# Kernel tuning notes

Hardware: AMD Instinct MI355X
Metric: run time of the kernel (lower is better)

Reference implementation:

```python
import jax, jax.numpy as jnp
import numpy as np
import math

N = 50000
E = 800000
D_IN, D_HID, D_OUT = 128, 64, 64
NUM_LAYERS = 8
ALPHA, THETA = 0.1, 0.5


def setup_inputs() -> dict:
    key = jax.random.key(0)
    ks = jax.random.split(key, 8)
    x = jax.random.normal(ks[0], (N, D_IN), dtype=jnp.float32)
    edge_index = jax.random.randint(ks[1], (2, E), 0, N, dtype=jnp.int64)
    s = 1.0 / np.sqrt(D_HID)
    W0 = jax.random.normal(ks[2], (D_IN, D_HID), dtype=jnp.float32) / np.sqrt(D_IN)
    b0 = jnp.zeros((D_HID,), dtype=jnp.float32)
    Ws = jax.random.normal(ks[3], (NUM_LAYERS, D_HID, D_HID), dtype=jnp.float32) * s
    W_out = jax.random.normal(ks[4], (D_HID, D_OUT), dtype=jnp.float32) * s
    b_out = jnp.zeros((D_OUT,), dtype=jnp.float32)
    return {"x": x, "edge_index": edge_index, "W0": W0, "b0": b0,
            "Ws": Ws, "W_out": W_out, "b_out": b_out}


def reference(x, edge_index, W0, b0, Ws, W_out, b_out):
    n = x.shape[0]
    # GCN normalization with self-loops (PyG gcn_norm, add_self_loops=True)
    loop = jnp.arange(n, dtype=edge_index.dtype)
    src = jnp.concatenate([edge_index[0], loop])
    dst = jnp.concatenate([edge_index[1], loop])
    ones = jnp.ones(src.shape[0], dtype=x.dtype)
    deg = jax.ops.segment_sum(ones, dst, num_segments=n)
    dinv = jnp.where(deg > 0, deg ** -0.5, 0.0)
    norm = (dinv[src] * dinv[dst])[:, None]  # [E+N, 1]

    def propagate(h):
        # out[i] = sum_{(j->i)} norm_ji * h[j]
        return jax.ops.segment_sum(norm * h[src], dst, num_segments=n)

    h = jax.nn.relu(x @ W0 + b0)
    h0 = h
    for layer in range(NUM_LAYERS):
        beta = math.log(THETA / (layer + 1) + 1.0)
        ah = propagate(h)
        xx = (1.0 - ALPHA) * ah + ALPHA * h0          # residual to x_0
        h = (1.0 - beta) * xx + beta * (xx @ Ws[layer])  # identity-mapped linear (shared weights)
        h = jax.nn.relu(h)
    return h @ W_out + b_out
```

## Files before the change

kernel.cpp:

```cpp
#include <hip/hip_runtime.h>
#include <hip/hip_fp16.h>
#include <math.h>

#define NN 50000
#define NE 800000
#define NLAYERS 8
#define NTILE (NN / 16)
#define EPB (NE / 256)
#define NBUCKB ((NN + 255) / 256)
#define BCAP 5120
#define CSRCAP 512

typedef _Float16 f16x8 __attribute__((ext_vector_type(8)));
typedef float f32x4 __attribute__((ext_vector_type(4)));


__global__ __launch_bounds__(256) void k_hist(const int* __restrict__ ei,
                                              int* __restrict__ gh) {
    __shared__ int h[256];
    h[threadIdx.x] = 0;
    __syncthreads();
    int base = blockIdx.x * EPB;
    for (int i = threadIdx.x; i < EPB; i += 256) {
        int d = __builtin_nontemporal_load(ei + NE + base + i);
        atomicAdd(&h[d >> 8], 1);
    }
    __syncthreads();
    gh[blockIdx.x * 256 + threadIdx.x] = h[threadIdx.x];
}

__global__ void k_scanhist(int* __restrict__ gh, int* __restrict__ bbase) {
    __shared__ int tot[256];
    int t = threadIdx.x;
    int run = 0;
    for (int blk = 0; blk < 256; blk++) {
        int v = gh[blk * 256 + t];
        gh[blk * 256 + t] = run;
        run += v;
    }
    tot[t] = run;
    __syncthreads();
    for (int off = 1; off < 256; off <<= 1) {
        int u = (t >= off) ? tot[t - off] : 0;
        __syncthreads();
        tot[t] += u;
        __syncthreads();
    }
    int ebase = tot[t] - run;
    for (int blk = 0; blk < 256; blk++) gh[blk * 256 + t] += ebase;
    bbase[t] = ebase;
    if (t == 255) bbase[256] = NE;
}

__global__ __launch_bounds__(256) void k_part(const int* __restrict__ ei,
                                              const int* __restrict__ gh,
                                              int2* __restrict__ part) {
    __shared__ int lcnt[256];
    int t = threadIdx.x;
    lcnt[t] = gh[blockIdx.x * 256 + t];
    __syncthreads();
    int base = blockIdx.x * EPB;
    for (int i = t; i < EPB; i += 256) {
        int s = __builtin_nontemporal_load(ei + base + i);
        int d = __builtin_nontemporal_load(ei + NE + base + i);
        int pos = atomicAdd(&lcnt[d >> 8], 1);
        int2 e; e.x = s; e.y = d;
        part[pos] = e;
    }
}

__global__ __launch_bounds__(256) void k_bsort(const int2* __restrict__ part,
                                               const int* __restrict__ bbase,
                                               int* __restrict__ csrs,
                                               int* __restrict__ offs,
                                               float* __restrict__ dinv,
                                               float* __restrict__ rdinv) {
    __shared__ int ssrc[BCAP];
    __shared__ unsigned char sdlo[BCAP];
    __shared__ int dcnt[256], dpos[256], scan[256];
    int b = blockIdx.x, t = threadIdx.x;
    int base0 = bbase[b], base1 = bbase[b + 1];
    int n = base1 - base0;
    if (n > BCAP) n = BCAP;
    dcnt[t] = 0;
    __syncthreads();
    for (int i = t; i < n; i += 256) {
        int2 e = part[base0 + i];
        ssrc[i] = e.x;
        int dlo = e.y & 255;
        sdlo[i] = (unsigned char)dlo;
        atomicAdd(&dcnt[dlo], 1);
    }
    __syncthreads();
    int cnt = dcnt[t];
    scan[t] = cnt;
    __syncthreads();
    for (int off = 1; off < 256; off <<= 1) {
        int u = (t >= off) ? scan[t - off] : 0;
        __syncthreads();
        scan[t] += u;
        __syncthreads();
    }
    int ebase = scan[t] - cnt;
    dpos[t] = ebase;
    __syncthreads();
    for (int i = t; i < n; i += 256) {
        int d = sdlo[i];
        int r = atomicAdd(&dpos[d], 1);
        csrs[base0 + r] = ssrc[i];
    }
    int gdst = b * 256 + t;
    if (gdst < NN) {
        offs[gdst] = base0 + ebase;
        float dd = (float)(cnt + 1);
        dinv[gdst] = rsqrtf(dd);
        rdinv[gdst] = sqrtf(dd);
    } else if (gdst == NN) {
        offs[NN] = NE;
    }
}


__global__ void k_zrow(__half2* a, __half2* b) {
    int t = threadIdx.x;
    __half2 z = __floats2half2_rn(0.f, 0.f);
    if (t < 32) a[NN * 32 + t] = z;
    else b[NN * 32 + (t & 31)] = z;
}

__global__ void k_makefrag(const float* __restrict__ W0, const float* __restrict__ Ws,
                           const float* __restrict__ Wout, __half* __restrict__ frag) {
    int fid = blockIdx.x;
    int lane = threadIdx.x;
    int m = lane & 15, g = lane >> 4;
#pragma unroll
    for (int j = 0; j < 8; j++) {
        float v;
        if (fid < 16) {
            int kt = fid >> 2, nb = fid & 3;
            int k = kt * 32 + g * 8 + j, n = nb * 16 + m;
            v = W0[k * 64 + n];
        } else if (fid < 80) {
            int t = fid - 16;
            int l = t >> 3, kt = (t >> 2) & 1, nb = t & 3;
            float beta = logf(0.5f / (float)(l + 1) + 1.0f);
            int k = kt * 32 + g * 8 + j, n = nb * 16 + m;
            v = beta * Ws[l * 4096 + k * 64 + n] + ((k == n) ? (1.0f - beta) : 0.0f);
        } else {
            int t = fid - 80;
            int kt = t >> 2, nb = t & 3;
            int k = kt * 32 + g * 8 + j, n = nb * 16 + m;
            v = Wout[k * 64 + n];
        }
        frag[fid * 512 + lane * 8 + j] = __float2half(v);
    }
}


__global__ __launch_bounds__(256) void k_layer0(const float* __restrict__ x,
        const __half* __restrict__ frag, const float* __restrict__ b0,
        const float* __restrict__ dinv,
        char* __restrict__ pbuf, char* __restrict__ h0buf) {
    __shared__ __half lds[4][16 * 80];
    int lane = threadIdx.x & 63, wave = threadIdx.x >> 6;
    int gwave = blockIdx.x * 4 + wave, nwaves = gridDim.x * 4;
    int m = lane & 15, g = lane >> 4;
    f16x8 bf[4][4];
    const int4* fb = (const int4*)frag;
#pragma unroll
    for (int kt = 0; kt < 4; kt++)
#pragma unroll
        for (int nb = 0; nb < 4; nb++) {
            int4 r = fb[(kt * 4 + nb) * 64 + lane];
            bf[kt][nb] = *(f16x8*)&r;
        }
    float bb[4];
#pragma unroll
    for (int nb = 0; nb < 4; nb++) bb[nb] = b0[nb * 16 + m];
    __half* L = &lds[wave][0];
    for (int t = gwave; t < NTILE; t += nwaves) {
        int tb = t * 16;
        f32x4 acc[4] = {};
        const float* xrow = x + (size_t)(tb + m) * 128;
#pragma unroll
        for (int kt = 0; kt < 4; kt++) {
            float4 r0 = *(const float4*)(xrow + kt * 32 + g * 8);
            float4 r1 = *(const float4*)(xrow + kt * 32 + g * 8 + 4);
            f16x8 af;
            af[0] = (_Float16)r0.x; af[1] = (_Float16)r0.y;
            af[2] = (_Float16)r0.z; af[3] = (_Float16)r0.w;
            af[4] = (_Float16)r1.x; af[5] = (_Float16)r1.y;
            af[6] = (_Float16)r1.z; af[7] = (_Float16)r1.w;
#pragma unroll
            for (int nb = 0; nb < 4; nb++)
                acc[nb] = __builtin_amdgcn_mfma_f32_16x16x32_f16(af, bf[kt][nb], acc[nb], 0, 0, 0);
        }
#pragma unroll
        for (int nb = 0; nb < 4; nb++)
#pragma unroll
            for (int r = 0; r < 4; r++) {
                int mm = g * 4 + r;
                float y = fmaxf(acc[nb][r] + bb[nb], 0.f);
                L[mm * 80 + nb * 16 + m] = __float2half(y);
            }
        asm volatile("" ::: "memory");
        int n2 = tb + m;
        float dv = dinv[n2];
        int4 lo = *(const int4*)&L[m * 80 + g * 8];
        int4 hi = *(const int4*)&L[m * 80 + 32 + g * 8];
        *(int4*)(h0buf + (size_t)n2 * 128 + g * 16) = lo;
        *(int4*)(h0buf + (size_t)n2 * 128 + 64 + g * 16) = hi;
        int4 slo, shi;
        const __half2* l2 = (const __half2*)&lo; __half2* s2 = (__half2*)&slo;
        const __half2* h2 = (const __half2*)&hi; __half2* t2 = (__half2*)&shi;
#pragma unroll
        for (int u = 0; u < 4; u++) {
            float2 a = __half22float2(l2[u]); s2[u] = __floats2half2_rn(a.x * dv, a.y * dv);
            float2 b = __half22float2(h2[u]); t2[u] = __floats2half2_rn(b.x * dv, b.y * dv);
        }
        *(int4*)(pbuf + (size_t)n2 * 128 + g * 16) = slo;
        *(int4*)(pbuf + (size_t)n2 * 128 + 64 + g * 16) = shi;
        asm volatile("" ::: "memory");
    }
}

__global__ __launch_bounds__(256) void k_flayer(
        const char* __restrict__ pbuf, const char* __restrict__ h0buf,
        const float* __restrict__ dinv, const __half* __restrict__ frag,
        const int* __restrict__ offs, const int* __restrict__ csrs,
        char* __restrict__ pout) {
    __shared__ int    csrl[4][CSRCAP];
    __shared__ __half aggl[4][16 * 72];
    __shared__ __half outl[4][16 * 80];
    int lane = threadIdx.x & 63, wave = threadIdx.x >> 6;
    int t = blockIdx.x * 4 + wave;
    if (t >= NTILE) return;
    int tb = t * 16;
    int m = lane & 15, g = lane >> 4;

    f16x8 bf[2][4];
    const int4* fb = (const int4*)frag;
#pragma unroll
    for (int kt = 0; kt < 2; kt++)
#pragma unroll
        for (int nb = 0; nb < 4; nb++) {
            int4 r = fb[(kt * 4 + nb) * 64 + lane];
            bf[kt][nb] = *(f16x8*)&r;
        }

    int offv = 0;
    if (lane < 17) offv = offs[tb + lane];
    int base = __shfl(offv, 0);
    int tot  = __shfl(offv, 16) - base;
    if (tot > CSRCAP) tot = CSRCAP;
    int* cl = csrl[wave];
    for (int i = lane; i < tot; i += 64)
        cl[i] = __builtin_nontemporal_load(csrs + base + i);

    int q = lane >> 4, s = (lane >> 3) & 1, fq = lane & 7;
    char* al = (char*)&aggl[wave][0];
#pragma unroll 1
    for (int p = 0; p < 4; p++) {
        int r0 = __shfl(offv, 4 * p + q) - base + s;
        int r1 = __shfl(offv, 4 * p + q + 1) - base;
        __half2 a0 = __floats2half2_rn(0.f, 0.f), a1 = a0, a2 = a0, a3 = a0;
#define GCH(IT) {                                                              \
        int idx = r0 + 2 * (IT);                                               \
        bool v = idx < r1;                                                     \
        int src = cl[v ? idx : 0];                                             \
        src = v ? src : NN;                                                    \
        int4 gld = *(const int4*)(pbuf + (size_t)src * 128 + fq * 16);         \
        a0 = __hadd2(a0, ((const __half2*)&gld)[0]);                           \
        a1 = __hadd2(a1, ((const __half2*)&gld)[1]);                           \
        a2 = __hadd2(a2, ((const __half2*)&gld)[2]);                           \
        a3 = __hadd2(a3, ((const __half2*)&gld)[3]); }
        GCH(0) GCH(1) GCH(2) GCH(3)
        int it = 4;
        while (__any(r0 + 2 * it < r1)) {
            GCH(it) GCH(it + 1)
            it += 2;
        }
#undef GCH
        a0 = __hadd2(a0, __shfl_xor(a0, 8));
        a1 = __hadd2(a1, __shfl_xor(a1, 8));
        a2 = __hadd2(a2, __shfl_xor(a2, 8));
        a3 = __hadd2(a3, __shfl_xor(a3, 8));
        if (s == 0) {
            int4 v;
            v.x = *(int*)&a0; v.y = *(int*)&a1; v.z = *(int*)&a2; v.w = *(int*)&a3;
            *(int4*)(al + (4 * p + q) * 144 + fq * 16) = v;
        }
    }
    asm volatile("" ::: "memory");

    float di = dinv[tb + m];
    float c9 = 0.9f * di;
    f32x4 acc[4] = {};
#pragma unroll
    for (int kt = 0; kt < 2; kt++) {
        int4 ra = *(const int4*)(al + m * 144 + kt * 64 + g * 16);
        int4 rp = *(const int4*)(pbuf + (size_t)(tb + m) * 128 + kt * 64 + g * 16);
        int4 rh = *(const int4*)(h0buf + (size_t)(tb + m) * 128 + kt * 64 + g * 16);
        f16x8 af;
#pragma unroll
        for (int u = 0; u < 4; u++) {
            float2 fa = __half22float2(((const __half2*)&ra)[u]);
            float2 fp = __half22float2(((const __half2*)&rp)[u]);
            float2 fh = __half22float2(((const __half2*)&rh)[u]);
            af[2 * u]     = (_Float16)(c9 * (fa.x + fp.x) + 0.1f * fh.x);
            af[2 * u + 1] = (_Float16)(c9 * (fa.y + fp.y) + 0.1f * fh.y);
        }
#pragma unroll
        for (int nb = 0; nb < 4; nb++)
            acc[nb] = __builtin_amdgcn_mfma_f32_16x16x32_f16(af, bf[kt][nb], acc[nb], 0, 0, 0);
    }

    __half* L = &outl[wave][0];
    float dvr[4];
#pragma unroll
    for (int r = 0; r < 4; r++) dvr[r] = dinv[tb + g * 4 + r];
#pragma unroll
    for (int nb = 0; nb < 4; nb++)
#pragma unroll
        for (int r = 0; r < 4; r++) {
            int mm = g * 4 + r;
            float y = fmaxf(acc[nb][r], 0.f) * dvr[r];
            L[mm * 80 + nb * 16 + m] = __float2half(y);
        }
    asm volatile("" ::: "memory");
    int n2 = tb + m;
    int4 lo = *(const int4*)&L[m * 80 + g * 8];
    int4 hi = *(const int4*)&L[m * 80 + 32 + g * 8];
    *(int4*)(pout + (size_t)n2 * 128 + g * 16) = lo;
    *(int4*)(pout + (size_t)n2 * 128 + 64 + g * 16) = hi;
}

__global__ __launch_bounds__(256) void k_out(const char* __restrict__ pbuf,
        const float* __restrict__ rdinv, const __half* __restrict__ frag,
        const float* __restrict__ bout, float* __restrict__ out) {
    __shared__ float lds[4][16 * 72];
    int lane = threadIdx.x & 63, wave = threadIdx.x >> 6;
    int gwave = blockIdx.x * 4 + wave, nwaves = gridDim.x * 4;
    int m = lane & 15, g = lane >> 4;
    f16x8 bf[2][4];
    const int4* fb = (const int4*)(frag + 80 * 512);
#pragma unroll
    for (int kt = 0; kt < 2; kt++)
#pragma unroll
        for (int nb = 0; nb < 4; nb++) {
            int4 r = fb[(kt * 4 + nb) * 64 + lane];
            bf[kt][nb] = *(f16x8*)&r;
        }
    float bb[4];
#pragma unroll
    for (int nb = 0; nb < 4; nb++) bb[nb] = bout[nb * 16 + m];
    float* L = &lds[wave][0];
    for (int t = gwave; t < NTILE; t += nwaves) {
        int tb = t * 16;
        float rv = rdinv[tb + m];
        f32x4 acc[4] = {};
#pragma unroll
        for (int kt = 0; kt < 2; kt++) {
            int4 rp = *(const int4*)(pbuf + (size_t)(tb + m) * 128 + kt * 64 + g * 16);
            f16x8 af;
#pragma unroll
            for (int u = 0; u < 4; u++) {
                float2 fp = __half22float2(((const __half2*)&rp)[u]);
                af[2 * u]     = (_Float16)(fp.x * rv);
                af[2 * u + 1] = (_Float16)(fp.y * rv);
            }
#pragma unroll
            for (int nb = 0; nb < 4; nb++)
                acc[nb] = __builtin_amdgcn_mfma_f32_16x16x32_f16(af, bf[kt][nb], acc[nb], 0, 0, 0);
        }
#pragma unroll
        for (int nb = 0; nb < 4; nb++)
#pragma unroll
            for (int r = 0; r < 4; r++)
                L[(g * 4 + r) * 72 + nb * 16 + m] = acc[nb][r] + bb[nb];
        asm volatile("" ::: "memory");
#pragma unroll
        for (int pass = 0; pass < 4; pass++) {
            int nl = pass * 4 + g;
            float4 v = *(const float4*)&L[nl * 72 + m * 4];
            *(float4*)(out + (size_t)(tb + nl) * 64 + m * 4) = v;
        }
        asm volatile("" ::: "memory");
    }
}


static inline size_t al256(size_t x) { return (x + 255) & ~(size_t)255; }

extern "C" void kernel_launch(void* const* d_in, const int* in_sizes, int n_in,
                              void* d_out, int out_size, void* d_ws, size_t ws_size,
                              hipStream_t stream) {
    const float* x    = (const float*)d_in[0];
    const int*   ei   = (const int*)d_in[1];
    const float* W0   = (const float*)d_in[2];
    const float* b0   = (const float*)d_in[3];
    const float* Ws   = (const float*)d_in[4];
    const float* Wout = (const float*)d_in[5];
    const float* bout = (const float*)d_in[6];
    float* out = (float*)d_out;

    char* w = (char*)d_ws;
    size_t off = 0;
    const size_t ROWS = (size_t)(NN + 1) * 128;
    int* gh      = (int*)(w + off); off = al256(off + (size_t)256 * 256 * 4);
    int* bbase   = (int*)(w + off); off = al256(off + (size_t)257 * 4);
    int2* part   = (int2*)(w + off); off = al256(off + (size_t)NE * 8);
    int* csrs    = (int*)(w + off); off = al256(off + ((size_t)NE + 256) * 4);
    int* offs    = (int*)(w + off); off = al256(off + ((size_t)NN + 1) * 4);
    float* dinv  = (float*)(w + off); off = al256(off + (size_t)NN * 4);
    float* rdinv = (float*)(w + off); off = al256(off + (size_t)NN * 4);
    __half* frag = (__half*)(w + off); off = al256(off + (size_t)88 * 512 * 2);
    char* pA     = (char*)(w + off); off = al256(off + ROWS);
    char* pB     = (char*)(w + off); off = al256(off + ROWS);
    char* h0b    = (char*)(w + off); off = al256(off + (size_t)NN * 128);

    k_hist<<<256, 256, 0, stream>>>(ei, gh);
    k_scanhist<<<1, 256, 0, stream>>>(gh, bbase);
    k_part<<<256, 256, 0, stream>>>(ei, gh, part);
    k_bsort<<<NBUCKB, 256, 0, stream>>>(part, bbase, csrs, offs, dinv, rdinv);
    k_zrow<<<1, 64, 0, stream>>>((__half2*)pA, (__half2*)pB);
    k_makefrag<<<88, 64, 0, stream>>>(W0, Ws, Wout, frag);

    k_layer0<<<784, 256, 0, stream>>>(x, frag, b0, dinv, pA, h0b);

    const char* cur = pA;
    char* nxt = pB;
    for (int l = 0; l < NLAYERS; l++) {
        k_flayer<<<(NTILE + 3) / 4, 256, 0, stream>>>(cur, h0b, dinv,
                frag + (16 + l * 8) * 512, offs, csrs, nxt);
        char* t2 = nxt;
        nxt = (char*)cur;
        cur = t2;
    }
    k_out<<<784, 256, 0, stream>>>(cur, rdinv, frag, bout, out);
}
```

Before: 227.6 us.

## Split each tile's edge gather across two waves and drop zero-row padding

Each 16-node tile in the propagate layer is now handled by two waves that interleave over the edge list, doubling the gathers in flight per tile and halving per-wave latency chains. Partial sums go to separate shared buffers, and after a block barrier one wave combines them and runs the MFMA transform. Out-of-range edges are now skipped with a branch instead of reading a zeroed sentinel row, so the k_zrow launch is removed. The cost is block-wide syncs, idle waves during the MFMA epilogue, and more divergence in the gather loop.

```diff
diff --git a/kernel.cpp b/kernel.cpp
--- a/kernel.cpp
+++ b/kernel.cpp
@@ -120,13 +120,6 @@
     }
 }
 
-
-__global__ void k_zrow(__half2* a, __half2* b) {
-    int t = threadIdx.x;
-    __half2 z = __floats2half2_rn(0.f, 0.f);
-    if (t < 32) a[NN * 32 + t] = z;
-    else b[NN * 32 + (t & 31)] = z;
-}
 
 __global__ void k_makefrag(const float* __restrict__ W0, const float* __restrict__ Ws,
                            const float* __restrict__ Wout, __half* __restrict__ frag) {
@@ -229,12 +222,14 @@
         const float* __restrict__ dinv, const __half* __restrict__ frag,
         const int* __restrict__ offs, const int* __restrict__ csrs,
         char* __restrict__ pout) {
-    __shared__ int    csrl[4][CSRCAP];
-    __shared__ __half aggl[4][16 * 72];
-    __shared__ __half outl[4][16 * 80];
+    __shared__ int    csrl[2][CSRCAP];
+    __shared__ __half aggl[2][2][16 * 72];
+    __shared__ __half outl[2][16 * 80];
     int lane = threadIdx.x & 63, wave = threadIdx.x >> 6;
-    int t = blockIdx.x * 4 + wave;
-    if (t >= NTILE) return;
+    int tpar = wave >> 1;
+    int b    = wave & 1;
+    int t = blockIdx.x * 2 + tpar;
+    bool valid = t < NTILE;
     int tb = t * 16;
     int m = lane & 15, g = lane >> 4;
 
@@ -249,73 +244,85 @@
         }
 
     int offv = 0;
-    if (lane < 17) offv = offs[tb + lane];
+    if (valid && lane < 17) offv = offs[tb + lane];
     int base = __shfl(offv, 0);
-    int tot  = __shfl(offv, 16) - base;
+    int tot  = valid ? (__shfl(offv, 16) - base) : 0;
     if (tot > CSRCAP) tot = CSRCAP;
-    int* cl = csrl[wave];
-    for (int i = lane; i < tot; i += 64)
+    int* cl = csrl[tpar];
+    for (int i = lane + b * 64; i < tot; i += 128)
         cl[i] = __builtin_nontemporal_load(csrs + base + i);
-
-    int q = lane >> 4, s = (lane >> 3) & 1, fq = lane & 7;
-    char* al = (char*)&aggl[wave][0];
+    __syncthreads();
+
+    if (valid) {
+        int q = lane >> 4;
+        int s = (lane >> 3) & 1;
+        int fq = lane & 7;
+        int slot = b * 2 + s;
+        char* al = (char*)&aggl[tpar][b][0];
 #pragma unroll 1
-    for (int p = 0; p < 4; p++) {
-        int r0 = __shfl(offv, 4 * p + q) - base + s;
-        int r1 = __shfl(offv, 4 * p + q + 1) - base;
-        __half2 a0 = __floats2half2_rn(0.f, 0.f), a1 = a0, a2 = a0, a3 = a0;
+        for (int p = 0; p < 4; p++) {
+            int r0 = __shfl(offv, 4 * p + q) - base + slot;
+            int r1 = __shfl(offv, 4 * p + q + 1) - base;
+            __half2 a0 = __floats2half2_rn(0.f, 0.f), a1 = a0, a2 = a0, a3 = a0;
 #define GCH(IT) {                                                              \
-        int idx = r0 + 2 * (IT);                                               \
-        bool v = idx < r1;                                                     \
-        int src = cl[v ? idx : 0];                                             \
-        src = v ? src : NN;                                                    \
-        int4 gld = *(const int4*)(pbuf + (size_t)src * 128 + fq * 16);         \
-        a0 = __hadd2(a0, ((const __half2*)&gld)[0]);                           \
-        a1 = __hadd2(a1, ((const __half2*)&gld)[1]);                           \
-        a2 = __hadd2(a2, ((const __half2*)&gld)[2]);                           \
-        a3 = __hadd2(a3, ((const __half2*)&gld)[3]); }
-        GCH(0) GCH(1) GCH(2) GCH(3)
-        int it = 4;
-        while (__any(r0 + 2 * it < r1)) {
-            GCH(it) GCH(it + 1)
-            it += 2;
-        }
+            int idx = r0 + 4 * (IT);                                           \
+            if (idx < r1) {                                                    \
+                int src = cl[idx];                                             \
+                int4 gld = *(const int4*)(pbuf + (size_t)src * 128 + fq * 16); \
+                a0 = __hadd2(a0, ((const __half2*)&gld)[0]);                   \
+                a1 = __hadd2(a1, ((const __half2*)&gld)[1]);                   \
+                a2 = __hadd2(a2, ((const __half2*)&gld)[2]);                   \
+                a3 = __hadd2(a3, ((const __half2*)&gld)[3]);                   \
+            } }
+            GCH(0) GCH(1) GCH(2) GCH(3)
+            int it = 4;
+            while (__any(r0 + 4 * it < r1)) {
+                GCH(it) GCH(it + 1)
+                it += 2;
+            }
 #undef GCH
-        a0 = __hadd2(a0, __shfl_xor(a0, 8));
-        a1 = __hadd2(a1, __shfl_xor(a1, 8));
-        a2 = __hadd2(a2, __shfl_xor(a2, 8));
-        a3 = __hadd2(a3, __shfl_xor(a3, 8));
-        if (s == 0) {
-            int4 v;
-            v.x = *(int*)&a0; v.y = *(int*)&a1; v.z = *(int*)&a2; v.w = *(int*)&a3;
-            *(int4*)(al + (4 * p + q) * 144 + fq * 16) = v;
-        }
-    }
-    asm volatile("" ::: "memory");
-
+            a0 = __hadd2(a0, __shfl_xor(a0, 8));
+            a1 = __hadd2(a1, __shfl_xor(a1, 8));
+            a2 = __hadd2(a2, __shfl_xor(a2, 8));
+            a3 = __hadd2(a3, __shfl_xor(a3, 8));
+            if (s == 0) {
+                int4 v;
+                v.x = *(int*)&a0; v.y = *(int*)&a1; v.z = *(int*)&a2; v.w = *(int*)&a3;
+                *(int4*)(al + (4 * p + q) * 144 + fq * 16) = v;
+            }
+        }
+    }
+    __syncthreads();
+
+    if (!valid || b) return;
+
+    const char* al0 = (const char*)&aggl[tpar][0][0];
+    const char* al1 = (const char*)&aggl[tpar][1][0];
     float di = dinv[tb + m];
     float c9 = 0.9f * di;
     f32x4 acc[4] = {};
 #pragma unroll
     for (int kt = 0; kt < 2; kt++) {
-        int4 ra = *(const int4*)(al + m * 144 + kt * 64 + g * 16);
+        int4 ra0 = *(const int4*)(al0 + m * 144 + kt * 64 + g * 16);
+        int4 ra1 = *(const int4*)(al1 + m * 144 + kt * 64 + g * 16);
         int4 rp = *(const int4*)(pbuf + (size_t)(tb + m) * 128 + kt * 64 + g * 16);
         int4 rh = *(const int4*)(h0buf + (size_t)(tb + m) * 128 + kt * 64 + g * 16);
         f16x8 af;
 #pragma unroll
         for (int u = 0; u < 4; u++) {
-            float2 fa = __half22float2(((const __half2*)&ra)[u]);
+            float2 f0 = __half22float2(((const __half2*)&ra0)[u]);
+            float2 f1 = __half22float2(((const __half2*)&ra1)[u]);
             float2 fp = __half22float2(((const __half2*)&rp)[u]);
             float2 fh = __half22float2(((const __half2*)&rh)[u]);
-            af[2 * u]     = (_Float16)(c9 * (fa.x + fp.x) + 0.1f * fh.x);
-            af[2 * u + 1] = (_Float16)(c9 * (fa.y + fp.y) + 0.1f * fh.y);
+            af[2 * u]     = (_Float16)(c9 * (f0.x + f1.x + fp.x) + 0.1f * fh.x);
+            af[2 * u + 1] = (_Float16)(c9 * (f0.y + f1.y + fp.y) + 0.1f * fh.y);
         }
 #pragma unroll
         for (int nb = 0; nb < 4; nb++)
             acc[nb] = __builtin_amdgcn_mfma_f32_16x16x32_f16(af, bf[kt][nb], acc[nb], 0, 0, 0);
     }
 
-    __half* L = &outl[wave][0];
+    __half* L = &outl[tpar][0];
     float dvr[4];
 #pragma unroll
     for (int r = 0; r < 4; r++) dvr[r] = dinv[tb + g * 4 + r];
@@ -423,7 +430,6 @@
     k_scanhist<<<1, 256, 0, stream>>>(gh, bbase);
     k_part<<<256, 256, 0, stream>>>(ei, gh, part);
     k_bsort<<<NBUCKB, 256, 0, stream>>>(part, bbase, csrs, offs, dinv, rdinv);
-    k_zrow<<<1, 64, 0, stream>>>((__half2*)pA, (__half2*)pB);
     k_makefrag<<<88, 64, 0, stream>>>(W0, Ws, Wout, frag);
 
     k_layer0<<<784, 256, 0, stream>>>(x, frag, b0, dinv, pA, h0b);
@@ -431,7 +437,7 @@
     const char* cur = pA;
     char* nxt = pB;
     for (int l = 0; l < NLAYERS; l++) {
-        k_flayer<<<(NTILE + 3) / 4, 256, 0, stream>>>(cur, h0b, dinv,
+        k_flayer<<<(NTILE + 1) / 2, 256, 0, stream>>>(cur, h0b, dinv,
                 frag + (16 + l * 8) * 512, offs, csrs, nxt);
         char* t2 = nxt;
         nxt = (char*)cur;
```

After: 300.2 us. 1.32x slower.

## Split each row's neighbor list by source panel to localize gathers

Applied to the files above, without the earlier changes.

The bucket sort now keys edges by destination and by whether the source index falls in the lower or upper half of the node range, and records a per-row split offset. The layer kernel gathers all low-panel neighbors for the tile's 16 rows first, then all high-panel neighbors, keeping four sets of accumulators in registers. The aim is to confine the random gather working set to half the feature table at a time so it hits cache more often. In exchange it adds an extra offsets array, more live registers, and a second divergent loop per row.

```diff
diff --git a/kernel.cpp b/kernel.cpp
--- a/kernel.cpp
+++ b/kernel.cpp
@@ -10,6 +10,7 @@
 #define NBUCKB ((NN + 255) / 256)
 #define BCAP 5120
 #define CSRCAP 512
+#define PANEL 25000
 
 typedef _Float16 f16x8 __attribute__((ext_vector_type(8)));
 typedef float f32x4 __attribute__((ext_vector_type(4)));
@@ -73,46 +74,49 @@
                                                const int* __restrict__ bbase,
                                                int* __restrict__ csrs,
                                                int* __restrict__ offs,
+                                               int* __restrict__ offp,
                                                float* __restrict__ dinv,
                                                float* __restrict__ rdinv) {
     __shared__ int ssrc[BCAP];
-    __shared__ unsigned char sdlo[BCAP];
-    __shared__ int dcnt[256], dpos[256], scan[256];
+    __shared__ unsigned short skey[BCAP];
+    __shared__ int dcnt[512], dpos[512];
+    __shared__ int pscan[256];
     int b = blockIdx.x, t = threadIdx.x;
     int base0 = bbase[b], base1 = bbase[b + 1];
     int n = base1 - base0;
     if (n > BCAP) n = BCAP;
-    dcnt[t] = 0;
+    dcnt[t] = 0; dcnt[t + 256] = 0;
     __syncthreads();
     for (int i = t; i < n; i += 256) {
         int2 e = part[base0 + i];
         ssrc[i] = e.x;
-        int dlo = e.y & 255;
-        sdlo[i] = (unsigned char)dlo;
-        atomicAdd(&dcnt[dlo], 1);
-    }
-    __syncthreads();
-    int cnt = dcnt[t];
-    scan[t] = cnt;
+        int key = ((e.y & 255) << 1) | (e.x >= PANEL ? 1 : 0);
+        skey[i] = (unsigned short)key;
+        atomicAdd(&dcnt[key], 1);
+    }
+    __syncthreads();
+    int c0 = dcnt[2 * t], c1 = dcnt[2 * t + 1];
+    pscan[t] = c0 + c1;
     __syncthreads();
     for (int off = 1; off < 256; off <<= 1) {
-        int u = (t >= off) ? scan[t - off] : 0;
+        int u = (t >= off) ? pscan[t - off] : 0;
         __syncthreads();
-        scan[t] += u;
+        pscan[t] += u;
         __syncthreads();
     }
-    int ebase = scan[t] - cnt;
-    dpos[t] = ebase;
+    int excl = pscan[t] - (c0 + c1);
+    dpos[2 * t] = excl;
+    dpos[2 * t + 1] = excl + c0;
     __syncthreads();
     for (int i = t; i < n; i += 256) {
-        int d = sdlo[i];
-        int r = atomicAdd(&dpos[d], 1);
+        int r = atomicAdd(&dpos[skey[i]], 1);
         csrs[base0 + r] = ssrc[i];
     }
     int gdst = b * 256 + t;
     if (gdst < NN) {
-        offs[gdst] = base0 + ebase;
-        float dd = (float)(cnt + 1);
+        offs[gdst] = base0 + excl;
+        offp[gdst] = base0 + excl + c0;
+        float dd = (float)(c0 + c1 + 1);
         dinv[gdst] = rsqrtf(dd);
         rdinv[gdst] = sqrtf(dd);
     } else if (gdst == NN) {
@@ -227,8 +231,8 @@
 __global__ __launch_bounds__(256) void k_flayer(
         const char* __restrict__ pbuf, const char* __restrict__ h0buf,
         const float* __restrict__ dinv, const __half* __restrict__ frag,
-        const int* __restrict__ offs, const int* __restrict__ csrs,
-        char* __restrict__ pout) {
+        const int* __restrict__ offs, const int* __restrict__ offp,
+        const int* __restrict__ csrs, char* __restrict__ pout) {
     __shared__ int    csrl[4][CSRCAP];
     __shared__ __half aggl[4][16 * 72];
     __shared__ __half outl[4][16 * 80];
@@ -248,43 +252,67 @@
             bf[kt][nb] = *(f16x8*)&r;
         }
 
-    int offv = 0;
+    int offv = 0, offpv = 0;
     if (lane < 17) offv = offs[tb + lane];
+    if (lane < 16) offpv = offp[tb + lane];
     int base = __shfl(offv, 0);
     int tot  = __shfl(offv, 16) - base;
     if (tot > CSRCAP) tot = CSRCAP;
     int* cl = csrl[wave];
     for (int i = lane; i < tot; i += 64)
         cl[i] = __builtin_nontemporal_load(csrs + base + i);
+    asm volatile("" ::: "memory");
 
     int q = lane >> 4, s = (lane >> 3) & 1, fq = lane & 7;
-    char* al = (char*)&aggl[wave][0];
-#pragma unroll 1
+    __half2 A0[4], A1[4], A2[4], A3[4];
+#pragma unroll
     for (int p = 0; p < 4; p++) {
-        int r0 = __shfl(offv, 4 * p + q) - base + s;
-        int r1 = __shfl(offv, 4 * p + q + 1) - base;
-        __half2 a0 = __floats2half2_rn(0.f, 0.f), a1 = a0, a2 = a0, a3 = a0;
-#define GCH(IT) {                                                              \
-        int idx = r0 + 2 * (IT);                                               \
-        bool v = idx < r1;                                                     \
+        A0[p] = __floats2half2_rn(0.f, 0.f);
+        A1[p] = A0[p]; A2[p] = A0[p]; A3[p] = A0[p];
+    }
+
+#define GCH(P, IDX, R1) {                                                      \
+        int idx = (IDX);                                                       \
+        bool v = idx < (R1);                                                   \
         int src = cl[v ? idx : 0];                                             \
         src = v ? src : NN;                                                    \
         int4 gld = *(const int4*)(pbuf + (size_t)src * 128 + fq * 16);         \
-        a0 = __hadd2(a0, ((const __half2*)&gld)[0]);                           \
-        a1 = __hadd2(a1, ((const __half2*)&gld)[1]);                           \
-        a2 = __hadd2(a2, ((const __half2*)&gld)[2]);                           \
-        a3 = __hadd2(a3, ((const __half2*)&gld)[3]); }
-        GCH(0) GCH(1) GCH(2) GCH(3)
-        int it = 4;
-        while (__any(r0 + 2 * it < r1)) {
-            GCH(it) GCH(it + 1)
-            it += 2;
-        }
+        A0[P] = __hadd2(A0[P], ((const __half2*)&gld)[0]);                     \
+        A1[P] = __hadd2(A1[P], ((const __half2*)&gld)[1]);                     \
+        A2[P] = __hadd2(A2[P], ((const __half2*)&gld)[2]);                     \
+        A3[P] = __hadd2(A3[P], ((const __half2*)&gld)[3]); }
+
+#pragma unroll
+    for (int p = 0; p < 4; p++) {
+        int r0 = __shfl(offv, 4 * p + q) - base + s;
+        int r1 = __shfl(offpv, 4 * p + q) - base;
+        GCH(p, r0, r1) GCH(p, r0 + 2, r1)
+        int it = r0 + 4;
+        while (__any(it < r1)) {
+            GCH(p, it, r1) GCH(p, it + 2, r1)
+            it += 4;
+        }
+    }
+#pragma unroll
+    for (int p = 0; p < 4; p++) {
+        int r0 = __shfl(offpv, 4 * p + q) - base + s;
+        int r1 = __shfl(offv, 4 * p + q + 1) - base;
+        GCH(p, r0, r1) GCH(p, r0 + 2, r1)
+        int it = r0 + 4;
+        while (__any(it < r1)) {
+            GCH(p, it, r1) GCH(p, it + 2, r1)
+            it += 4;
+        }
+    }
 #undef GCH
-        a0 = __hadd2(a0, __shfl_xor(a0, 8));
-        a1 = __hadd2(a1, __shfl_xor(a1, 8));
-        a2 = __hadd2(a2, __shfl_xor(a2, 8));
-        a3 = __hadd2(a3, __shfl_xor(a3, 8));
+
+    char* al = (char*)&aggl[wave][0];
+#pragma unroll
+    for (int p = 0; p < 4; p++) {
+        __half2 a0 = __hadd2(A0[p], __shfl_xor(A0[p], 8));
+        __half2 a1 = __hadd2(A1[p], __shfl_xor(A1[p], 8));
+        __half2 a2 = __hadd2(A2[p], __shfl_xor(A2[p], 8));
+        __half2 a3 = __hadd2(A3[p], __shfl_xor(A3[p], 8));
         if (s == 0) {
             int4 v;
             v.x = *(int*)&a0; v.y = *(int*)&a1; v.z = *(int*)&a2; v.w = *(int*)&a3;
@@ -412,6 +440,7 @@
     int2* part   = (int2*)(w + off); off = al256(off + (size_t)NE * 8);
     int* csrs    = (int*)(w + off); off = al256(off + ((size_t)NE + 256) * 4);
     int* offs    = (int*)(w + off); off = al256(off + ((size_t)NN + 1) * 4);
+    int* offp    = (int*)(w + off); off = al256(off + (size_t)NN * 4);
     float* dinv  = (float*)(w + off); off = al256(off + (size_t)NN * 4);
     float* rdinv = (float*)(w + off); off = al256(off + (size_t)NN * 4);
     __half* frag = (__half*)(w + off); off = al256(off + (size_t)88 * 512 * 2);
@@ -422,7 +451,7 @@
     k_hist<<<256, 256, 0, stream>>>(ei, gh);
     k_scanhist<<<1, 256, 0, stream>>>(gh, bbase);
     k_part<<<256, 256, 0, stream>>>(ei, gh, part);
-    k_bsort<<<NBUCKB, 256, 0, stream>>>(part, bbase, csrs, offs, dinv, rdinv);
+    k_bsort<<<NBUCKB, 256, 0, stream>>>(part, bbase, csrs, offs, offp, dinv, rdinv);
     k_zrow<<<1, 64, 0, stream>>>((__half2*)pA, (__half2*)pB);
     k_makefrag<<<88, 64, 0, stream>>>(W0, Ws, Wout, frag);
 
@@ -432,7 +461,7 @@
     char* nxt = pB;
     for (int l = 0; l < NLAYERS; l++) {
         k_flayer<<<(NTILE + 3) / 4, 256, 0, stream>>>(cur, h0b, dinv,
-                frag + (16 + l * 8) * 512, offs, csrs, nxt);
+                frag + (16 + l * 8) * 512, offs, offp, csrs, nxt);
         char* t2 = nxt;
         nxt = (char*)cur;
         cur = t2;
```

Measured after the change: 304.0 us. +33.6%, slower.

## Renumber nodes by in-degree so gather tiles have uniform degree

Applied to the files above, without the earlier changes.

Adds a counting sort of nodes by in-degree (capped at 63 bins) and renumbers nodes, the CSR, the normalisation arrays and the feature buffers into that order. Each 16-node gather tile then holds nodes of similar degree, which is meant to cut wave divergence and idle lanes in the neighbour-gather loop. Tile indices are also scrambled with a multiplicative permutation to spread heavy and light tiles across blocks, and the LDS CSR cache is enlarged. The cost is extra preprocessing kernels, including a serial per-node remap, and a scattered write at the output. The offset formula assumes in-degree is at most 63, so nodes with higher degree would get wrong offsets.

```diff
diff --git a/kernel.cpp b/kernel.cpp
--- a/kernel.cpp
+++ b/kernel.cpp
@@ -9,7 +9,7 @@
 #define EPB (NE / 256)
 #define NBUCKB ((NN + 255) / 256)
 #define BCAP 5120
-#define CSRCAP 512
+#define CSRCAP 768
 
 typedef _Float16 f16x8 __attribute__((ext_vector_type(8)));
 typedef float f32x4 __attribute__((ext_vector_type(4)));
@@ -118,6 +118,72 @@
     } else if (gdst == NN) {
         offs[NN] = NE;
     }
+}
+
+
+__global__ __launch_bounds__(256) void k_deghist(const int* __restrict__ offs,
+                                                 int* __restrict__ dh) {
+    __shared__ int h[64];
+    if (threadIdx.x < 64) h[threadIdx.x] = 0;
+    __syncthreads();
+    int i = blockIdx.x * 256 + threadIdx.x;
+    if (i < NN) {
+        int d = offs[i + 1] - offs[i];
+        if (d > 63) d = 63;
+        atomicAdd(&h[d], 1);
+    }
+    __syncthreads();
+    if (threadIdx.x < 64) atomicAdd(&dh[threadIdx.x], h[threadIdx.x]);
+}
+
+__global__ void k_degscan(const int* __restrict__ dh, int* __restrict__ dbase,
+                          int* __restrict__ ebase, int* __restrict__ binpos) {
+    __shared__ int sc[64], se[64];
+    int t = threadIdx.x;
+    int c = dh[t];
+    sc[t] = c;
+    se[t] = c * t;
+    __syncthreads();
+    for (int off = 1; off < 64; off <<= 1) {
+        int u = (t >= off) ? sc[t - off] : 0;
+        int v = (t >= off) ? se[t - off] : 0;
+        __syncthreads();
+        sc[t] += u; se[t] += v;
+        __syncthreads();
+    }
+    dbase[t] = sc[t] - c;
+    binpos[t] = sc[t] - c;
+    ebase[t] = se[t] - c * t;
+}
+
+__global__ __launch_bounds__(256) void k_rank(const int* __restrict__ offs,
+        int* __restrict__ binpos, const int* __restrict__ dbase,
+        const int* __restrict__ ebase,
+        const float* __restrict__ dinv, const float* __restrict__ rdinv,
+        int* __restrict__ rank, int* __restrict__ iperm, int* __restrict__ offsp,
+        float* __restrict__ dinvp, float* __restrict__ rdinvp) {
+    int i = blockIdx.x * 256 + threadIdx.x;
+    if (i >= NN) return;
+    int d = offs[i + 1] - offs[i];
+    if (d > 63) d = 63;
+    int r = atomicAdd(&binpos[d], 1);
+    rank[i] = r;
+    iperm[r] = i;
+    dinvp[r] = dinv[i];
+    rdinvp[r] = rdinv[i];
+    offsp[r] = ebase[d] + (r - dbase[d]) * d;
+    if (i == 0) offsp[NN] = NE;
+}
+
+__global__ __launch_bounds__(256) void k_remap(const int* __restrict__ offs,
+        const int* __restrict__ rank, const int* __restrict__ offsp,
+        const int* __restrict__ csrs, int* __restrict__ csrs2) {
+    int i = blockIdx.x * 256 + threadIdx.x;
+    if (i >= NN) return;
+    int b = offs[i], e = offs[i + 1];
+    int ob = offsp[rank[i]];
+    for (int k = b; k < e; k++)
+        csrs2[ob + (k - b)] = rank[csrs[k]];
 }
 
 
@@ -159,7 +225,7 @@
 
 __global__ __launch_bounds__(256) void k_layer0(const float* __restrict__ x,
         const __half* __restrict__ frag, const float* __restrict__ b0,
-        const float* __restrict__ dinv,
+        const float* __restrict__ dinv, const int* __restrict__ rank,
         char* __restrict__ pbuf, char* __restrict__ h0buf) {
     __shared__ __half lds[4][16 * 80];
     int lane = threadIdx.x & 63, wave = threadIdx.x >> 6;
@@ -206,10 +272,11 @@
         asm volatile("" ::: "memory");
         int n2 = tb + m;
         float dv = dinv[n2];
+        int rr = rank[n2];
         int4 lo = *(const int4*)&L[m * 80 + g * 8];
         int4 hi = *(const int4*)&L[m * 80 + 32 + g * 8];
-        *(int4*)(h0buf + (size_t)n2 * 128 + g * 16) = lo;
-        *(int4*)(h0buf + (size_t)n2 * 128 + 64 + g * 16) = hi;
+        *(int4*)(h0buf + (size_t)rr * 128 + g * 16) = lo;
+        *(int4*)(h0buf + (size_t)rr * 128 + 64 + g * 16) = hi;
         int4 slo, shi;
         const __half2* l2 = (const __half2*)&lo; __half2* s2 = (__half2*)&slo;
         const __half2* h2 = (const __half2*)&hi; __half2* t2 = (__half2*)&shi;
@@ -218,23 +285,24 @@
             float2 a = __half22float2(l2[u]); s2[u] = __floats2half2_rn(a.x * dv, a.y * dv);
             float2 b = __half22float2(h2[u]); t2[u] = __floats2half2_rn(b.x * dv, b.y * dv);
         }
-        *(int4*)(pbuf + (size_t)n2 * 128 + g * 16) = slo;
-        *(int4*)(pbuf + (size_t)n2 * 128 + 64 + g * 16) = shi;
+        *(int4*)(pbuf + (size_t)rr * 128 + g * 16) = slo;
+        *(int4*)(pbuf + (size_t)rr * 128 + 64 + g * 16) = shi;
         asm volatile("" ::: "memory");
     }
 }
 
 __global__ __launch_bounds__(256) void k_flayer(
         const char* __restrict__ pbuf, const char* __restrict__ h0buf,
-        const float* __restrict__ dinv, const __half* __restrict__ frag,
-        const int* __restrict__ offs, const int* __restrict__ csrs,
+        const float* __restrict__ dinvp, const __half* __restrict__ frag,
+        const int* __restrict__ offsp, const int* __restrict__ csrs2,
         char* __restrict__ pout) {
     __shared__ int    csrl[4][CSRCAP];
     __shared__ __half aggl[4][16 * 72];
     __shared__ __half outl[4][16 * 80];
     int lane = threadIdx.x & 63, wave = threadIdx.x >> 6;
-    int t = blockIdx.x * 4 + wave;
-    if (t >= NTILE) return;
+    int t0 = blockIdx.x * 4 + wave;
+    if (t0 >= NTILE) return;
+    int t = (int)(((long long)t0 * 1563) % NTILE);
     int tb = t * 16;
     int m = lane & 15, g = lane >> 4;
 
@@ -249,13 +317,13 @@
         }
 
     int offv = 0;
-    if (lane < 17) offv = offs[tb + lane];
+    if (lane < 17) offv = offsp[tb + lane];
     int base = __shfl(offv, 0);
     int tot  = __shfl(offv, 16) - base;
     if (tot > CSRCAP) tot = CSRCAP;
     int* cl = csrl[wave];
     for (int i = lane; i < tot; i += 64)
-        cl[i] = __builtin_nontemporal_load(csrs + base + i);
+        cl[i] = __builtin_nontemporal_load(csrs2 + base + i);
 
     int q = lane >> 4, s = (lane >> 3) & 1, fq = lane & 7;
     char* al = (char*)&aggl[wave][0];
@@ -293,7 +361,7 @@
     }
     asm volatile("" ::: "memory");
 
-    float di = dinv[tb + m];
+    float di = dinvp[tb + m];
     float c9 = 0.9f * di;
     f32x4 acc[4] = {};
 #pragma unroll
@@ -318,7 +386,7 @@
     __half* L = &outl[wave][0];
     float dvr[4];
 #pragma unroll
-    for (int r = 0; r < 4; r++) dvr[r] = dinv[tb + g * 4 + r];
+    for (int r = 0; r < 4; r++) dvr[r] = dinvp[tb + g * 4 + r];
 #pragma unroll
     for (int nb = 0; nb < 4; nb++)
 #pragma unroll
@@ -336,7 +404,8 @@
 }
 
 __global__ __launch_bounds__(256) void k_out(const char* __restrict__ pbuf,
-        const float* __restrict__ rdinv, const __half* __restrict__ frag,
+        const float* __restrict__ rdinvp, const int* __restrict__ iperm,
+        const __half* __restrict__ frag,
         const float* __restrict__ bout, float* __restrict__ out) {
     __shared__ float lds[4][16 * 72];
     int lane = threadIdx.x & 63, wave = threadIdx.x >> 6;
@@ -357,7 +426,7 @@
     float* L = &lds[wave][0];
     for (int t = gwave; t < NTILE; t += nwaves) {
         int tb = t * 16;
-        float rv = rdinv[tb + m];
+        float rv = rdinvp[tb + m];
         f32x4 acc[4] = {};
 #pragma unroll
         for (int kt = 0; kt < 2; kt++) {
@@ -382,8 +451,9 @@
 #pragma unroll
         for (int pass = 0; pass < 4; pass++) {
             int nl = pass * 4 + g;
+            int onode = iperm[tb + nl];
             float4 v = *(const float4*)&L[nl * 72 + m * 4];
-            *(float4*)(out + (size_t)(tb + nl) * 64 + m * 4) = v;
+            *(float4*)(out + (size_t)onode * 64 + m * 4) = v;
         }
         asm volatile("" ::: "memory");
     }
@@ -411,31 +481,48 @@
     int* bbase   = (int*)(w + off); off = al256(off + (size_t)257 * 4);
     int2* part   = (int2*)(w + off); off = al256(off + (size_t)NE * 8);
     int* csrs    = (int*)(w + off); off = al256(off + ((size_t)NE + 256) * 4);
+    int* csrs2   = (int*)(w + off); off = al256(off + ((size_t)NE + 256) * 4);
     int* offs    = (int*)(w + off); off = al256(off + ((size_t)NN + 1) * 4);
+    int* offsp   = (int*)(w + off); off = al256(off + ((size_t)NN + 1) * 4);
+    int* rank    = (int*)(w + off); off = al256(off + (size_t)NN * 4);
+    int* iperm   = (int*)(w + off); off = al256(off + (size_t)NN * 4);
     float* dinv  = (float*)(w + off); off = al256(off + (size_t)NN * 4);
     float* rdinv = (float*)(w + off); off = al256(off + (size_t)NN * 4);
+    float* dinvp = (float*)(w + off); off = al256(off + (size_t)NN * 4);
+    float* rdinvp= (float*)(w + off); off = al256(off + (size_t)NN * 4);
+    int* dh      = (int*)(w + off); off = al256(off + (size_t)64 * 4);
+    int* dbase   = (int*)(w + off); off = al256(off + (size_t)64 * 4);
+    int* ebase   = (int*)(w + off); off = al256(off + (size_t)64 * 4);
+    int* binpos  = (int*)(w + off); off = al256(off + (size_t)64 * 4);
     __half* frag = (__half*)(w + off); off = al256(off + (size_t)88 * 512 * 2);
     char* pA     = (char*)(w + off); off = al256(off + ROWS);
     char* pB     = (char*)(w + off); off = al256(off + ROWS);
     char* h0b    = (char*)(w + off); off = al256(off + (size_t)NN * 128);
 
+    hipMemsetAsync(dh, 0, 64 * 4, stream);
+
     k_hist<<<256, 256, 0, stream>>>(ei, gh);
     k_scanhist<<<1, 256, 0, stream>>>(gh, bbase);
     k_part<<<256, 256, 0, stream>>>(ei, gh, part);
     k_bsort<<<NBUCKB, 256, 0, stream>>>(part, bbase, csrs, offs, dinv, rdinv);
+    k_deghist<<<NBUCKB, 256, 0, stream>>>(offs, dh);
+    k_degscan<<<1, 64, 0, stream>>>(dh, dbase, ebase, binpos);
+    k_rank<<<NBUCKB, 256, 0, stream>>>(offs, binpos, dbase, ebase, dinv, rdinv,
+                                       rank, iperm, offsp, dinvp, rdinvp);
+    k_remap<<<NBUCKB, 256, 0, stream>>>(offs, rank, offsp, csrs, csrs2);
     k_zrow<<<1, 64, 0, stream>>>((__half2*)pA, (__half2*)pB);
     k_makefrag<<<88, 64, 0, stream>>>(W0, Ws, Wout, frag);
 
-    k_layer0<<<784, 256, 0, stream>>>(x, frag, b0, dinv, pA, h0b);
+    k_layer0<<<784, 256, 0, stream>>>(x, frag, b0, dinv, rank, pA, h0b);
 
     const char* cur = pA;
     char* nxt = pB;
     for (int l = 0; l < NLAYERS; l++) {
-        k_flayer<<<(NTILE + 3) / 4, 256, 0, stream>>>(cur, h0b, dinv,
-                frag + (16 + l * 8) * 512, offs, csrs, nxt);
+        k_flayer<<<(NTILE + 3) / 4, 256, 0, stream>>>(cur, h0b, dinvp,
+                frag + (16 + l * 8) * 512, offsp, csrs2, nxt);
         char* t2 = nxt;
         nxt = (char*)cur;
         cur = t2;
     }
-    k_out<<<784, 256, 0, stream>>>(cur, rdinv, frag, bout, out);
-}
+    k_out<<<784, 256, 0, stream>>>(cur, rdinvp, iperm, frag, bout, out);
+}
```

Result: slower. 421.4 us (+85.2%).
